# Performance work log

Hardware: AMD Instinct MI355X
Metric: run time of the kernel (lower is better)

Reference implementation:

```python
import jax, jax.numpy as jnp
import numpy as np
import math

S, D, H, DK, DV, FF = 128, 512, 8, 64, 64, 2048

def _pos_encoding(S, D):
    pos = jnp.arange(S, dtype=jnp.float32)[:, None]                      # [S,1]
    div = jnp.exp(jnp.arange(0, D, 2, dtype=jnp.float32) * (-math.log(10000.0) / D))
    pe = jnp.zeros((S, D), dtype=jnp.float32)
    pe = pe.at[:, 0::2].set(jnp.sin(pos * div))
    pe = pe.at[:, 1::2].set(jnp.cos(pos * div))
    return pe

def setup_inputs():
    key = jax.random.key(0)
    ks = jax.random.split(key, 16)
    B = 512
    return {
        'x':      jax.random.normal(ks[0], (B, S, D), dtype=jnp.float32),
        'emb_w':  jax.random.normal(ks[1], (D, D), dtype=jnp.float32) * 0.02,
        'emb_b':  jnp.zeros((D,), dtype=jnp.float32),
        'WQ':     jax.random.uniform(ks[2], (H, D, DK), dtype=jnp.float32) * 0.05,
        'WK':     jax.random.uniform(ks[3], (H, D, DK), dtype=jnp.float32) * 0.05,
        'WV':     jax.random.uniform(ks[4], (H, D, DV), dtype=jnp.float32) * 0.05,
        'WO':     jax.random.uniform(ks[5], (H * DV, D), dtype=jnp.float32) * 0.05,
        'norm_w': jnp.ones((S, D), dtype=jnp.float32),
        'norm_b': jnp.zeros((S, D), dtype=jnp.float32),
        'l1_w':   jax.random.normal(ks[6], (D, FF), dtype=jnp.float32) * 0.02,
        'l1_b':   jnp.zeros((FF,), dtype=jnp.float32),
        'l2_w':   jax.random.normal(ks[7], (FF, D), dtype=jnp.float32) * 0.02,
        'l2_b':   jnp.zeros((D,), dtype=jnp.float32),
        'fc_w':   jax.random.normal(ks[8], (256, 2), dtype=jnp.float32) * 0.05,
        'fc_b':   jnp.zeros((2,), dtype=jnp.float32),
    }

def reference(x, emb_w, emb_b, WQ, WK, WV, WO, norm_w, norm_b, l1_w, l1_b, l2_w, l2_b, fc_w, fc_b):
    B = x.shape[0]
    h = x @ emb_w + emb_b                                   # [B,S,D] embedding linear
    h = h + _pos_encoding(S, D)[None]                       # add sinusoidal PE
    # multi-head attention (all heads batched in one einsum instead of the per-head python loop)
    q = jnp.einsum('bsd,hdk->bhsk', h, WQ)                  # [B,H,S,DK]
    k = jnp.einsum('bsd,hdk->bhsk', h, WK)
    v = jnp.einsum('bsd,hdv->bhsv', h, WV)
    scores = jnp.einsum('bhsk,bhtk->bhst', q, k) / math.sqrt(DK)
    attn = jax.nn.softmax(scores, axis=-1)                  # [B,H,S,S]
    o = jnp.einsum('bhst,bhtv->bhsv', attn, v)              # [B,H,S,DV]
    o = jnp.transpose(o, (0, 2, 1, 3)).reshape(B, S, H * DV)  # concat heads
    o = o @ WO                                              # [B,S,D]
    # residual (dropout is identity in eval) + LayerNorm over (S, D)
    r = o + h
    mu = jnp.mean(r, axis=(1, 2), keepdims=True)
    var = jnp.mean(jnp.square(r - mu), axis=(1, 2), keepdims=True)
    r = (r - mu) * jax.lax.rsqrt(var + 1e-5) * norm_w + norm_b
    # FFN
    f = jax.nn.relu(r @ l1_w + l1_b) @ l2_w + l2_b          # [B,S,D]
    # MaxPool2d(16,16) over (S,D): [B,S,D] -> [B,S/16,D/16]
    p = f.reshape(B, S // 16, 16, D // 16, 16).max(axis=(2, 4))  # [B,8,32]
    p = p.reshape(B, 256)
    logits = p @ fc_w + fc_b                                # [B,2]
    return jax.nn.log_softmax(logits, axis=-1)
```

## Files before the change

kernel.cpp:

```cpp
#include <hip/hip_runtime.h>
#include <hip/hip_bf16.h>
#include <cstdint>
#include <math.h>

#define NB 512
#define NS 128
#define ND 512
#define NH 8
#define NDK 64
#define NFF 2048

typedef __attribute__((ext_vector_type(4))) float f32x4;
typedef __attribute__((ext_vector_type(8))) short s16x8;

#define AS1 __attribute__((address_space(1)))
#define AS3 __attribute__((address_space(3)))

__device__ __forceinline__ ushort f2b(float f) {
  __hip_bfloat16 h = __float2bfloat16(f);
  return *reinterpret_cast<ushort*>(&h);
}
__device__ __forceinline__ float b2f(ushort u) {
  __hip_bfloat16 h;
  *reinterpret_cast<ushort*>(&h) = u;
  return __bfloat162float(h);
}
__device__ __forceinline__ void gll16(const void* g, void* l) {
  __builtin_amdgcn_global_load_lds(
      (const AS1 unsigned int*)g,
      reinterpret_cast<AS3 unsigned int*>(reinterpret_cast<uintptr_t>(l)),
      16, 0, 0);
}

__global__ void conv_bf16(const float* __restrict__ in, ushort* __restrict__ out, int n4) {
  int i = blockIdx.x * blockDim.x + threadIdx.x;
  if (i >= n4) return;
  float4 v = *(const float4*)(in + (size_t)i * 4);
  ushort4 o;
  o.x = f2b(v.x); o.y = f2b(v.y); o.z = f2b(v.z); o.w = f2b(v.w);
  *(ushort4*)(out + (size_t)i * 4) = o;
}

__global__ void pack_t(const float* __restrict__ in, ushort* __restrict__ out, int R, int C) {
  int i = blockIdx.x * blockDim.x + threadIdx.x;
  if (i >= R * C) return;
  int r = i / C, c = i - r * C;
  out[(size_t)c * R + r] = f2b(in[i]);
}

__global__ void pack_qkv(const float* __restrict__ WQ, const float* __restrict__ WK,
                         const float* __restrict__ WV, ushort* __restrict__ out) {
  int i = blockIdx.x * blockDim.x + threadIdx.x;
  if (i >= NH * 192 * ND) return;
  int h = i / (192 * ND);
  int rem = i - h * (192 * ND);
  int n = rem / ND, d = rem - n * ND;
  size_t base = (size_t)h * ND * NDK + (size_t)d * NDK;
  float v;
  if (n < 64)       v = WQ[base + n] * 0.125f;
  else if (n < 128) v = WK[base + (n - 64)];
  else              v = WV[base + (n - 128)];
  out[i] = f2b(v);
}

__global__ void pe_build(float* __restrict__ pe) {
  int i = blockIdx.x * blockDim.x + threadIdx.x;
  if (i >= NS * ND) return;
  int s = i >> 9, d = i & 511;
  float e = expf((float)(d & ~1) * (-9.210340371976184f / 512.f));
  float ang = (float)s * e;
  pe[i] = (d & 1) ? cosf(ang) : sinf(ang);
}

template <int EPI>
__global__ __launch_bounds__(256, 2) void gemm_bf16(
    const ushort* __restrict__ A, const ushort* __restrict__ Bt,
    int M, int N, int K,
    ushort* __restrict__ Obf, float* __restrict__ Of,
    const float* __restrict__ bias, const float* __restrict__ pe,
    const ushort* __restrict__ res, float* __restrict__ stats,
    float* __restrict__ pool) {
  __shared__ __align__(16) ushort lA[2][4096];
  __shared__ __align__(16) ushort lB[2][4096];
  const int tid = threadIdx.x, lane = tid & 63, wid = tid >> 6;
  const int wr = wid >> 1, wc = wid & 1;
  const int lo = lane & 15, hi = lane >> 4;
  const int ntil = N >> 7;
  const int bm = blockIdx.x / ntil, bn = blockIdx.x - bm * ntil;
  const int m0 = bm << 7, n0 = bn << 7;
  const int rr = lane >> 2, cc = (lane & 3) << 3;

  f32x4 acc[4][4];
#pragma unroll
  for (int m = 0; m < 4; ++m)
#pragma unroll
    for (int n = 0; n < 4; ++n) acc[m][n] = (f32x4){0.f, 0.f, 0.f, 0.f};

  const int nk = K >> 5;
  for (int s = wid; s < 8; s += 4) {
    gll16(&A[(size_t)(m0 + s * 16 + rr) * K + cc], &lA[0][s * 512]);
    gll16(&Bt[(size_t)(n0 + s * 16 + rr) * K + cc], &lB[0][s * 512]);
  }
  __syncthreads();
  for (int t = 0; t < nk; ++t) {
    const int cur = t & 1;
    if (t + 1 < nk) {
      const int k0 = (t + 1) << 5;
      for (int s = wid; s < 8; s += 4) {
        gll16(&A[(size_t)(m0 + s * 16 + rr) * K + k0 + cc], &lA[cur ^ 1][s * 512]);
        gll16(&Bt[(size_t)(n0 + s * 16 + rr) * K + k0 + cc], &lB[cur ^ 1][s * 512]);
      }
    }
    s16x8 af[4], bfr[4];
#pragma unroll
    for (int m = 0; m < 4; ++m)
      af[m] = *(const s16x8*)&lA[cur][(wr * 64 + m * 16 + lo) * 32 + hi * 8];
#pragma unroll
    for (int n = 0; n < 4; ++n)
      bfr[n] = *(const s16x8*)&lB[cur][(wc * 64 + n * 16 + lo) * 32 + hi * 8];
#pragma unroll
    for (int m = 0; m < 4; ++m)
#pragma unroll
      for (int n = 0; n < 4; ++n)
        acc[m][n] = __builtin_amdgcn_mfma_f32_16x16x32_bf16(af[m], bfr[n], acc[m][n], 0, 0, 0);
    __syncthreads();
  }

  if constexpr (EPI == 0) {
#pragma unroll
    for (int m = 0; m < 4; ++m)
#pragma unroll
      for (int n = 0; n < 4; ++n) {
        const int col = n0 + wc * 64 + n * 16 + lo;
        const float bv = bias[col];
#pragma unroll
        for (int j = 0; j < 4; ++j) {
          const int row = m0 + wr * 64 + m * 16 + hi * 4 + j;
          const float v = acc[m][n][j] + bv + pe[((row & 127) << 9) + col];
          Obf[(size_t)row * N + col] = f2b(v);
        }
      }
  } else if constexpr (EPI == 1) {
    float s1 = 0.f, s2 = 0.f;
#pragma unroll
    for (int m = 0; m < 4; ++m)
#pragma unroll
      for (int n = 0; n < 4; ++n) {
        const int col = n0 + wc * 64 + n * 16 + lo;
#pragma unroll
        for (int j = 0; j < 4; ++j) {
          const int row = m0 + wr * 64 + m * 16 + hi * 4 + j;
          const float v = acc[m][n][j] + b2f(res[(size_t)row * 512 + col]);
          Of[(size_t)row * 512 + col] = v;
          s1 += v; s2 += v * v;
        }
      }
    s1 += __shfl_xor(s1, 1);  s2 += __shfl_xor(s2, 1);
    s1 += __shfl_xor(s1, 2);  s2 += __shfl_xor(s2, 2);
    s1 += __shfl_xor(s1, 4);  s2 += __shfl_xor(s2, 4);
    s1 += __shfl_xor(s1, 8);  s2 += __shfl_xor(s2, 8);
    s1 += __shfl_xor(s1, 16); s2 += __shfl_xor(s2, 16);
    s1 += __shfl_xor(s1, 32); s2 += __shfl_xor(s2, 32);
    if (lane == 0) {
      atomicAdd(&stats[bm * 2], s1);
      atomicAdd(&stats[bm * 2 + 1], s2);
    }
  } else if constexpr (EPI == 2) {
#pragma unroll
    for (int m = 0; m < 4; ++m)
#pragma unroll
      for (int n = 0; n < 4; ++n) {
        const int col = n0 + wc * 64 + n * 16 + lo;
        const float bv = bias[col];
#pragma unroll
        for (int j = 0; j < 4; ++j) {
          const int row = m0 + wr * 64 + m * 16 + hi * 4 + j;
          Obf[(size_t)row * N + col] = f2b(fmaxf(acc[m][n][j] + bv, 0.f));
        }
      }
  } else {
#pragma unroll
    for (int m = 0; m < 4; ++m)
#pragma unroll
      for (int n = 0; n < 4; ++n) {
        const int col = n0 + wc * 64 + n * 16 + lo;
        float fv = fmaxf(fmaxf(acc[m][n][0], acc[m][n][1]),
                         fmaxf(acc[m][n][2], acc[m][n][3])) + bias[col];
        fv = fmaxf(fv, __shfl_xor(fv, 1));
        fv = fmaxf(fv, __shfl_xor(fv, 2));
        fv = fmaxf(fv, __shfl_xor(fv, 4));
        fv = fmaxf(fv, __shfl_xor(fv, 8));
        fv = fmaxf(fv, __shfl_xor(fv, 16));
        fv = fmaxf(fv, __shfl_xor(fv, 32));
        if (lane == 0)
          pool[bm * 256 + (wr * 4 + m) * 32 + (bn * 8 + wc * 4 + n)] = fv;
      }
  }
}

__global__ __launch_bounds__(256, 2) void attn_fused(
    const ushort* __restrict__ h, const ushort* __restrict__ wqkvT,
    ushort* __restrict__ o) {
  __shared__ __align__(16) ushort smem[32768];
  ushort* uni = smem;
  ushort* kb = smem + 16384;
  ushort* vT = smem + 24576;
  float* redm = (float*)(smem + 16384);
  float* reds = redm + 256;

  const int tid = threadIdx.x, lane = tid & 63, wid = tid >> 6;
  const int wr = wid >> 1, wc = wid & 1;
  const int lo = lane & 15, hi = lane >> 4;
  const int bh = blockIdx.x;
  const int b = bh >> 3, hd = bh & 7;
  const ushort* hsrc = h + (size_t)b * (NS * ND);
  const ushort* wsrc = wqkvT + (size_t)hd * (192 * ND);
  const int rr = lane >> 2, cc = (lane & 3) << 3;

  f32x4 a1[4][6];
#pragma unroll
  for (int m = 0; m < 4; ++m)
#pragma unroll
    for (int n = 0; n < 6; ++n) a1[m][n] = (f32x4){0.f, 0.f, 0.f, 0.f};
  for (int t = 0; t < 16; ++t) {
    const int k0 = t << 5;
    for (int s = wid; s < 8; s += 4)
      gll16(&hsrc[(size_t)(s * 16 + rr) * ND + k0 + cc], &uni[s * 512]);
    for (int s = wid; s < 12; s += 4)
      gll16(&wsrc[(size_t)(s * 16 + rr) * ND + k0 + cc], &uni[4096 + s * 512]);
    __syncthreads();
    s16x8 af[4], bfr[6];
#pragma unroll
    for (int m = 0; m < 4; ++m)
      af[m] = *(const s16x8*)&uni[(wr * 64 + m * 16 + lo) * 32 + hi * 8];
#pragma unroll
    for (int n = 0; n < 6; ++n)
      bfr[n] = *(const s16x8*)&uni[4096 + (wc * 96 + n * 16 + lo) * 32 + hi * 8];
#pragma unroll
    for (int m = 0; m < 4; ++m)
#pragma unroll
      for (int n = 0; n < 6; ++n)
        a1[m][n] = __builtin_amdgcn_mfma_f32_16x16x32_bf16(af[m], bfr[n], a1[m][n], 0, 0, 0);
    __syncthreads();
  }
#pragma unroll
  for (int m = 0; m < 4; ++m)
#pragma unroll
    for (int n = 0; n < 6; ++n)
#pragma unroll
      for (int j = 0; j < 4; ++j) {
        const int row = wr * 64 + m * 16 + hi * 4 + j;
        const int c = wc * 96 + n * 16 + lo;
        const ushort v = f2b(a1[m][n][j]);
        if (c < 64) uni[row * 64 + c] = v;
        else if (c < 128) kb[row * 64 + (c - 64)] = v;
        else vT[(c - 128) * 128 + row] = v;
      }
  __syncthreads();

  f32x4 sc[4][4];
#pragma unroll
  for (int m = 0; m < 4; ++m)
#pragma unroll
    for (int n = 0; n < 4; ++n) sc[m][n] = (f32x4){0.f, 0.f, 0.f, 0.f};
#pragma unroll
  for (int kt = 0; kt < 2; ++kt) {
    s16x8 aq[4], bk[4];
#pragma unroll
    for (int m = 0; m < 4; ++m)
      aq[m] = *(const s16x8*)&uni[(wr * 64 + m * 16 + lo) * 64 + kt * 32 + hi * 8];
#pragma unroll
    for (int n = 0; n < 4; ++n)
      bk[n] = *(const s16x8*)&kb[(wc * 64 + n * 16 + lo) * 64 + kt * 32 + hi * 8];
#pragma unroll
    for (int m = 0; m < 4; ++m)
#pragma unroll
      for (int n = 0; n < 4; ++n)
        sc[m][n] = __builtin_amdgcn_mfma_f32_16x16x32_bf16(aq[m], bk[n], sc[m][n], 0, 0, 0);
  }
  __syncthreads();

  float rmax[4][4];
#pragma unroll
  for (int m = 0; m < 4; ++m)
#pragma unroll
    for (int j = 0; j < 4; ++j) {
      float v = fmaxf(fmaxf(sc[m][0][j], sc[m][1][j]), fmaxf(sc[m][2][j], sc[m][3][j]));
      v = fmaxf(v, __shfl_xor(v, 1));
      v = fmaxf(v, __shfl_xor(v, 2));
      v = fmaxf(v, __shfl_xor(v, 4));
      v = fmaxf(v, __shfl_xor(v, 8));
      rmax[m][j] = v;
    }
  if (lo == 0) {
#pragma unroll
    for (int m = 0; m < 4; ++m)
#pragma unroll
      for (int j = 0; j < 4; ++j)
        redm[wc * 128 + wr * 64 + m * 16 + hi * 4 + j] = rmax[m][j];
  }
  __syncthreads();
  float rsum[4][4];
#pragma unroll
  for (int m = 0; m < 4; ++m)
#pragma unroll
    for (int j = 0; j < 4; ++j) {
      const int row = wr * 64 + m * 16 + hi * 4 + j;
      const float mx = fmaxf(redm[row], redm[128 + row]);
      float s = 0.f;
#pragma unroll
      for (int n = 0; n < 4; ++n) {
        const float p = __expf(sc[m][n][j] - mx);
        uni[row * 128 + wc * 64 + n * 16 + lo] = f2b(p);
        s += p;
      }
      s += __shfl_xor(s, 1);
      s += __shfl_xor(s, 2);
      s += __shfl_xor(s, 4);
      s += __shfl_xor(s, 8);
      rsum[m][j] = s;
    }
  if (lo == 0) {
#pragma unroll
    for (int m = 0; m < 4; ++m)
#pragma unroll
      for (int j = 0; j < 4; ++j)
        reds[wc * 128 + wr * 64 + m * 16 + hi * 4 + j] = rsum[m][j];
  }
  __syncthreads();
  float inv[4][4];
#pragma unroll
  for (int m = 0; m < 4; ++m)
#pragma unroll
    for (int j = 0; j < 4; ++j) {
      const int row = wr * 64 + m * 16 + hi * 4 + j;
      inv[m][j] = 1.f / (reds[row] + reds[128 + row]);
    }

  f32x4 oa[4][2];
#pragma unroll
  for (int m = 0; m < 4; ++m)
#pragma unroll
    for (int n = 0; n < 2; ++n) oa[m][n] = (f32x4){0.f, 0.f, 0.f, 0.f};
#pragma unroll
  for (int kt = 0; kt < 4; ++kt) {
    s16x8 ap[4], bv[2];
#pragma unroll
    for (int m = 0; m < 4; ++m)
      ap[m] = *(const s16x8*)&uni[(wr * 64 + m * 16 + lo) * 128 + kt * 32 + hi * 8];
#pragma unroll
    for (int n = 0; n < 2; ++n)
      bv[n] = *(const s16x8*)&vT[(wc * 32 + n * 16 + lo) * 128 + kt * 32 + hi * 8];
#pragma unroll
    for (int m = 0; m < 4; ++m)
#pragma unroll
      for (int n = 0; n < 2; ++n)
        oa[m][n] = __builtin_amdgcn_mfma_f32_16x16x32_bf16(ap[m], bv[n], oa[m][n], 0, 0, 0);
  }
#pragma unroll
  for (int m = 0; m < 4; ++m)
#pragma unroll
    for (int n = 0; n < 2; ++n)
#pragma unroll
      for (int j = 0; j < 4; ++j) {
        const int row = wr * 64 + m * 16 + hi * 4 + j;
        const int c = wc * 32 + n * 16 + lo;
        o[((size_t)b * NS + row) * ND + hd * 64 + c] = f2b(oa[m][n][j] * inv[m][j]);
      }
}

__global__ void ln_apply(const float* __restrict__ r, const float* __restrict__ stats,
                         const float* __restrict__ nw, const float* __restrict__ nb,
                         ushort* __restrict__ rn) {
  int i = blockIdx.x * blockDim.x + threadIdx.x;
  int base = i << 2;
  if (base >= NB * NS * ND) return;
  int b = base >> 16;
  int sd = base & 65535;
  float mu = stats[2 * b] * (1.f / 65536.f);
  float var = stats[2 * b + 1] * (1.f / 65536.f) - mu * mu;
  float rs = rsqrtf(var + 1e-5f);
  float4 rv = *(const float4*)(r + base);
  float4 w = *(const float4*)(nw + sd);
  float4 bb = *(const float4*)(nb + sd);
  ushort4 ov;
  ov.x = f2b((rv.x - mu) * rs * w.x + bb.x);
  ov.y = f2b((rv.y - mu) * rs * w.y + bb.y);
  ov.z = f2b((rv.z - mu) * rs * w.z + bb.z);
  ov.w = f2b((rv.w - mu) * rs * w.w + bb.w);
  *(ushort4*)(rn + base) = ov;
}

__global__ void fc_logsoftmax(const float* __restrict__ p, const float* __restrict__ w,
                              const float* __restrict__ bias, float* __restrict__ out) {
  int b = blockIdx.x * blockDim.x + threadIdx.x;
  if (b >= NB) return;
  float l0 = bias[0], l1 = bias[1];
  const float* pr = p + b * 256;
  for (int k = 0; k < 256; ++k) {
    float pv = pr[k];
    l0 += pv * w[2 * k];
    l1 += pv * w[2 * k + 1];
  }
  float mx = fmaxf(l0, l1);
  float lse = mx + logf(expf(l0 - mx) + expf(l1 - mx));
  out[2 * b] = l0 - lse;
  out[2 * b + 1] = l1 - lse;
}

extern "C" void kernel_launch(void* const* d_in, const int* in_sizes, int n_in,
                              void* d_out, int out_size, void* d_ws, size_t ws_size,
                              hipStream_t stream) {
  const float* x      = (const float*)d_in[0];
  const float* emb_w  = (const float*)d_in[1];
  const float* emb_b  = (const float*)d_in[2];
  const float* WQ     = (const float*)d_in[3];
  const float* WK     = (const float*)d_in[4];
  const float* WV     = (const float*)d_in[5];
  const float* WO     = (const float*)d_in[6];
  const float* norm_w = (const float*)d_in[7];
  const float* norm_b = (const float*)d_in[8];
  const float* l1_w   = (const float*)d_in[9];
  const float* l1_b   = (const float*)d_in[10];
  const float* l2_w   = (const float*)d_in[11];
  const float* l2_b   = (const float*)d_in[12];
  const float* fc_w   = (const float*)d_in[13];
  const float* fc_b   = (const float*)d_in[14];
  float* out = (float*)d_out;
  char* ws = (char*)d_ws;

  constexpr size_t MB = 1ull << 20;
  ushort* xb   = (ushort*)(ws + 0);
  ushort* hbuf = (ushort*)(ws + 64 * MB);
  ushort* obuf = (ushort*)(ws + 128 * MB);
  float*  rbuf = (float*)(ws + 192 * MB);
  ushort* f1   = (ushort*)(ws + 0);
  ushort* rnb  = (ushort*)(ws + 320 * MB);
  char* wb = ws + 384 * MB;
  ushort* embT  = (ushort*)(wb);
  ushort* woT   = (ushort*)(wb + 524288);
  ushort* l1T   = (ushort*)(wb + 1048576);
  ushort* l2T   = (ushort*)(wb + 3145728);
  ushort* wqkvT = (ushort*)(wb + 5242880);
  float*  peb   = (float*)(wb + 6815744);
  float*  stats = (float*)(wb + 7077888);
  float*  poolb = (float*)(wb + 7086080);

  hipMemsetAsync(stats, 0, NB * 2 * sizeof(float), stream);

  conv_bf16<<<32768, 256, 0, stream>>>(x, xb, NB * NS * ND / 4);
  pe_build<<<256, 256, 0, stream>>>(peb);
  pack_t<<<1024, 256, 0, stream>>>(emb_w, embT, 512, 512);
  pack_t<<<1024, 256, 0, stream>>>(WO, woT, 512, 512);
  pack_t<<<4096, 256, 0, stream>>>(l1_w, l1T, 512, 2048);
  pack_t<<<4096, 256, 0, stream>>>(l2_w, l2T, 2048, 512);
  pack_qkv<<<3072, 256, 0, stream>>>(WQ, WK, WV, wqkvT);

  gemm_bf16<0><<<2048, 256, 0, stream>>>(xb, embT, NB * NS, ND, ND,
                                         hbuf, nullptr, emb_b, peb, nullptr, nullptr, nullptr);
  attn_fused<<<NB * NH, 256, 0, stream>>>(hbuf, wqkvT, obuf);
  gemm_bf16<1><<<2048, 256, 0, stream>>>(obuf, woT, NB * NS, ND, ND,
                                         nullptr, rbuf, nullptr, nullptr, hbuf, stats, nullptr);
  ln_apply<<<32768, 256, 0, stream>>>(rbuf, stats, norm_w, norm_b, rnb);
  gemm_bf16<2><<<8192, 256, 0, stream>>>(rnb, l1T, NB * NS, NFF, ND,
                                         f1, nullptr, l1_b, nullptr, nullptr, nullptr, nullptr);
  gemm_bf16<3><<<2048, 256, 0, stream>>>(f1, l2T, NB * NS, ND, NFF,
                                         nullptr, nullptr, l2_b, nullptr, nullptr, nullptr, poolb);
  fc_logsoftmax<<<2, 256, 0, stream>>>(poolb, fc_w, fc_b, out);
}
```

Measured before the change: 1.054 ms.

## Split fused attention into QKV GEMM plus lightweight attention core kernel

The per-(batch,head) QKV projection moves out of the attention kernel into a separate full-tile GEMM with a new epilogue. That epilogue scatters Q, K and transposed V into per-head bf16 buffers in global memory. The attention kernel then only loads these tiles into XOR-swizzled shared memory, computes the scores with each wave owning full rows, and does the softmax without cross-wave reductions. This aims for better MFMA efficiency in the projection and higher occupancy in attention, at the cost of an extra global round trip for Q/K/V and reshuffled workspace aliasing.

```diff
diff --git a/kernel.cpp b/kernel.cpp
--- a/kernel.cpp
+++ b/kernel.cpp
@@ -178,7 +178,7 @@
           Obf[(size_t)row * N + col] = f2b(fmaxf(acc[m][n][j] + bv, 0.f));
         }
       }
-  } else {
+  } else if constexpr (EPI == 3) {
 #pragma unroll
     for (int m = 0; m < 4; ++m)
 #pragma unroll
@@ -195,177 +195,154 @@
         if (lane == 0)
           pool[bm * 256 + (wr * 4 + m) * 32 + (bn * 8 + wc * 4 + n)] = fv;
       }
-  }
-}
-
-__global__ __launch_bounds__(256, 2) void attn_fused(
-    const ushort* __restrict__ h, const ushort* __restrict__ wqkvT,
-    ushort* __restrict__ o) {
-  __shared__ __align__(16) ushort smem[32768];
-  ushort* uni = smem;
-  ushort* kb = smem + 16384;
-  ushort* vT = smem + 24576;
-  float* redm = (float*)(smem + 16384);
-  float* reds = redm + 256;
-
+  } else {
+    ushort* kbp = (ushort*)Of;
+    ushort* vtp = (ushort*)pool;
+#pragma unroll
+    for (int m = 0; m < 4; ++m)
+#pragma unroll
+      for (int n = 0; n < 4; ++n) {
+        const int cn0 = n0 + wc * 64 + n * 16;
+        const int h = cn0 / 192;
+        const int rem = cn0 - h * 192;
+        const int kind = rem >> 6;
+        const int idx = (rem & 63) + lo;
+#pragma unroll
+        for (int j = 0; j < 4; ++j) {
+          const int row = m0 + wr * 64 + m * 16 + hi * 4 + j;
+          const size_t hb = (size_t)((row >> 7) * 8 + h) * 8192;
+          const ushort v = f2b(acc[m][n][j]);
+          if (kind == 0)      Obf[hb + (row & 127) * 64 + idx] = v;
+          else if (kind == 1) kbp[hb + (row & 127) * 64 + idx] = v;
+          else                vtp[hb + (size_t)idx * 128 + (row & 127)] = v;
+        }
+      }
+  }
+}
+
+__global__ __launch_bounds__(256, 3) void attn_core(
+    const ushort* __restrict__ qb, const ushort* __restrict__ kb,
+    const ushort* __restrict__ vtb, ushort* __restrict__ o) {
+  __shared__ __align__(16) ushort smem[24576];
   const int tid = threadIdx.x, lane = tid & 63, wid = tid >> 6;
-  const int wr = wid >> 1, wc = wid & 1;
   const int lo = lane & 15, hi = lane >> 4;
   const int bh = blockIdx.x;
-  const int b = bh >> 3, hd = bh & 7;
-  const ushort* hsrc = h + (size_t)b * (NS * ND);
-  const ushort* wsrc = wqkvT + (size_t)hd * (192 * ND);
-  const int rr = lane >> 2, cc = (lane & 3) << 3;
-
-  f32x4 a1[4][6];
-#pragma unroll
-  for (int m = 0; m < 4; ++m)
-#pragma unroll
-    for (int n = 0; n < 6; ++n) a1[m][n] = (f32x4){0.f, 0.f, 0.f, 0.f};
-  for (int t = 0; t < 16; ++t) {
-    const int k0 = t << 5;
-    for (int s = wid; s < 8; s += 4)
-      gll16(&hsrc[(size_t)(s * 16 + rr) * ND + k0 + cc], &uni[s * 512]);
-    for (int s = wid; s < 12; s += 4)
-      gll16(&wsrc[(size_t)(s * 16 + rr) * ND + k0 + cc], &uni[4096 + s * 512]);
-    __syncthreads();
-    s16x8 af[4], bfr[6];
-#pragma unroll
-    for (int m = 0; m < 4; ++m)
-      af[m] = *(const s16x8*)&uni[(wr * 64 + m * 16 + lo) * 32 + hi * 8];
-#pragma unroll
-    for (int n = 0; n < 6; ++n)
-      bfr[n] = *(const s16x8*)&uni[4096 + (wc * 96 + n * 16 + lo) * 32 + hi * 8];
-#pragma unroll
-    for (int m = 0; m < 4; ++m)
-#pragma unroll
-      for (int n = 0; n < 6; ++n)
-        a1[m][n] = __builtin_amdgcn_mfma_f32_16x16x32_bf16(af[m], bfr[n], a1[m][n], 0, 0, 0);
-    __syncthreads();
-  }
-#pragma unroll
-  for (int m = 0; m < 4; ++m)
-#pragma unroll
-    for (int n = 0; n < 6; ++n)
-#pragma unroll
-      for (int j = 0; j < 4; ++j) {
-        const int row = wr * 64 + m * 16 + hi * 4 + j;
-        const int c = wc * 96 + n * 16 + lo;
-        const ushort v = f2b(a1[m][n][j]);
-        if (c < 64) uni[row * 64 + c] = v;
-        else if (c < 128) kb[row * 64 + (c - 64)] = v;
-        else vT[(c - 128) * 128 + row] = v;
-      }
+  const size_t base = (size_t)bh * 8192;
+
+#pragma unroll
+  for (int i = 0; i < 4; ++i) {
+    const int Lb = (wid * 4 + i) * 64;
+    const int L = Lb + lane;
+    {
+      const int r = L >> 3, c = L & 7;
+      gll16(&qb[base + r * 64 + ((c ^ (r & 7)) << 3)], &smem[Lb * 8]);
+      gll16(&kb[base + r * 64 + ((c ^ (r & 7)) << 3)], &smem[8192 + Lb * 8]);
+    }
+    {
+      const int r = L >> 4, c = L & 15;
+      gll16(&vtb[base + r * 128 + ((c ^ (r & 15)) << 3)], &smem[16384 + Lb * 8]);
+    }
+  }
   __syncthreads();
 
-  f32x4 sc[4][4];
-#pragma unroll
-  for (int m = 0; m < 4; ++m)
-#pragma unroll
-    for (int n = 0; n < 4; ++n) sc[m][n] = (f32x4){0.f, 0.f, 0.f, 0.f};
+  f32x4 sc[2][8];
+#pragma unroll
+  for (int m = 0; m < 2; ++m)
+#pragma unroll
+    for (int n = 0; n < 8; ++n) sc[m][n] = (f32x4){0.f, 0.f, 0.f, 0.f};
 #pragma unroll
   for (int kt = 0; kt < 2; ++kt) {
-    s16x8 aq[4], bk[4];
-#pragma unroll
-    for (int m = 0; m < 4; ++m)
-      aq[m] = *(const s16x8*)&uni[(wr * 64 + m * 16 + lo) * 64 + kt * 32 + hi * 8];
-#pragma unroll
-    for (int n = 0; n < 4; ++n)
-      bk[n] = *(const s16x8*)&kb[(wc * 64 + n * 16 + lo) * 64 + kt * 32 + hi * 8];
-#pragma unroll
-    for (int m = 0; m < 4; ++m)
-#pragma unroll
-      for (int n = 0; n < 4; ++n)
+    s16x8 aq[2], bk[8];
+#pragma unroll
+    for (int m = 0; m < 2; ++m) {
+      const int row = wid * 32 + m * 16 + lo;
+      aq[m] = *(const s16x8*)&smem[row * 64 + (((kt * 4 + hi) ^ (row & 7)) << 3)];
+    }
+#pragma unroll
+    for (int n = 0; n < 8; ++n) {
+      const int kr = n * 16 + lo;
+      bk[n] = *(const s16x8*)&smem[8192 + kr * 64 + (((kt * 4 + hi) ^ (kr & 7)) << 3)];
+    }
+#pragma unroll
+    for (int m = 0; m < 2; ++m)
+#pragma unroll
+      for (int n = 0; n < 8; ++n)
         sc[m][n] = __builtin_amdgcn_mfma_f32_16x16x32_bf16(aq[m], bk[n], sc[m][n], 0, 0, 0);
   }
   __syncthreads();
 
-  float rmax[4][4];
-#pragma unroll
-  for (int m = 0; m < 4; ++m)
+  float inv[2][4];
+#pragma unroll
+  for (int m = 0; m < 2; ++m)
 #pragma unroll
     for (int j = 0; j < 4; ++j) {
-      float v = fmaxf(fmaxf(sc[m][0][j], sc[m][1][j]), fmaxf(sc[m][2][j], sc[m][3][j]));
-      v = fmaxf(v, __shfl_xor(v, 1));
-      v = fmaxf(v, __shfl_xor(v, 2));
-      v = fmaxf(v, __shfl_xor(v, 4));
-      v = fmaxf(v, __shfl_xor(v, 8));
-      rmax[m][j] = v;
-    }
-  if (lo == 0) {
-#pragma unroll
-    for (int m = 0; m < 4; ++m)
-#pragma unroll
-      for (int j = 0; j < 4; ++j)
-        redm[wc * 128 + wr * 64 + m * 16 + hi * 4 + j] = rmax[m][j];
-  }
-  __syncthreads();
-  float rsum[4][4];
-#pragma unroll
-  for (int m = 0; m < 4; ++m)
-#pragma unroll
-    for (int j = 0; j < 4; ++j) {
-      const int row = wr * 64 + m * 16 + hi * 4 + j;
-      const float mx = fmaxf(redm[row], redm[128 + row]);
+      float mx = sc[m][0][j];
+#pragma unroll
+      for (int n = 1; n < 8; ++n) mx = fmaxf(mx, sc[m][n][j]);
+      mx = fmaxf(mx, __shfl_xor(mx, 1));
+      mx = fmaxf(mx, __shfl_xor(mx, 2));
+      mx = fmaxf(mx, __shfl_xor(mx, 4));
+      mx = fmaxf(mx, __shfl_xor(mx, 8));
       float s = 0.f;
 #pragma unroll
-      for (int n = 0; n < 4; ++n) {
+      for (int n = 0; n < 8; ++n) {
         const float p = __expf(sc[m][n][j] - mx);
-        uni[row * 128 + wc * 64 + n * 16 + lo] = f2b(p);
+        sc[m][n][j] = p;
         s += p;
       }
       s += __shfl_xor(s, 1);
       s += __shfl_xor(s, 2);
       s += __shfl_xor(s, 4);
       s += __shfl_xor(s, 8);
-      rsum[m][j] = s;
-    }
-  if (lo == 0) {
-#pragma unroll
-    for (int m = 0; m < 4; ++m)
-#pragma unroll
-      for (int j = 0; j < 4; ++j)
-        reds[wc * 128 + wr * 64 + m * 16 + hi * 4 + j] = rsum[m][j];
-  }
+      inv[m][j] = 1.f / s;
+    }
+#pragma unroll
+  for (int m = 0; m < 2; ++m)
+#pragma unroll
+    for (int n = 0; n < 8; ++n)
+#pragma unroll
+      for (int j = 0; j < 4; ++j) {
+        const int row = wid * 32 + m * 16 + hi * 4 + j;
+        const int col = n * 16 + lo;
+        smem[row * 128 + ((((col >> 3) ^ (row & 15)) << 3) | (col & 7))] =
+            f2b(sc[m][n][j]);
+      }
   __syncthreads();
-  float inv[4][4];
-#pragma unroll
-  for (int m = 0; m < 4; ++m)
-#pragma unroll
-    for (int j = 0; j < 4; ++j) {
-      const int row = wr * 64 + m * 16 + hi * 4 + j;
-      inv[m][j] = 1.f / (reds[row] + reds[128 + row]);
-    }
-
-  f32x4 oa[4][2];
-#pragma unroll
-  for (int m = 0; m < 4; ++m)
-#pragma unroll
-    for (int n = 0; n < 2; ++n) oa[m][n] = (f32x4){0.f, 0.f, 0.f, 0.f};
+
+  f32x4 oa[2][4];
+#pragma unroll
+  for (int m = 0; m < 2; ++m)
+#pragma unroll
+    for (int n = 0; n < 4; ++n) oa[m][n] = (f32x4){0.f, 0.f, 0.f, 0.f};
 #pragma unroll
   for (int kt = 0; kt < 4; ++kt) {
-    s16x8 ap[4], bv[2];
-#pragma unroll
-    for (int m = 0; m < 4; ++m)
-      ap[m] = *(const s16x8*)&uni[(wr * 64 + m * 16 + lo) * 128 + kt * 32 + hi * 8];
-#pragma unroll
-    for (int n = 0; n < 2; ++n)
-      bv[n] = *(const s16x8*)&vT[(wc * 32 + n * 16 + lo) * 128 + kt * 32 + hi * 8];
-#pragma unroll
-    for (int m = 0; m < 4; ++m)
-#pragma unroll
-      for (int n = 0; n < 2; ++n)
+    s16x8 ap[2], bv[4];
+#pragma unroll
+    for (int m = 0; m < 2; ++m) {
+      const int row = wid * 32 + m * 16 + lo;
+      ap[m] = *(const s16x8*)&smem[row * 128 + (((kt * 4 + hi) ^ (row & 15)) << 3)];
+    }
+#pragma unroll
+    for (int n = 0; n < 4; ++n) {
+      const int vr = n * 16 + lo;
+      bv[n] = *(const s16x8*)&smem[16384 + vr * 128 + (((kt * 4 + hi) ^ (vr & 15)) << 3)];
+    }
+#pragma unroll
+    for (int m = 0; m < 2; ++m)
+#pragma unroll
+      for (int n = 0; n < 4; ++n)
         oa[m][n] = __builtin_amdgcn_mfma_f32_16x16x32_bf16(ap[m], bv[n], oa[m][n], 0, 0, 0);
   }
-#pragma unroll
-  for (int m = 0; m < 4; ++m)
-#pragma unroll
-    for (int n = 0; n < 2; ++n)
+  const int b = bh >> 3, hd = bh & 7;
+#pragma unroll
+  for (int m = 0; m < 2; ++m)
+#pragma unroll
+    for (int n = 0; n < 4; ++n)
 #pragma unroll
       for (int j = 0; j < 4; ++j) {
-        const int row = wr * 64 + m * 16 + hi * 4 + j;
-        const int c = wc * 32 + n * 16 + lo;
-        o[((size_t)b * NS + row) * ND + hd * 64 + c] = f2b(oa[m][n][j] * inv[m][j]);
+        const int row = wid * 32 + m * 16 + hi * 4 + j;
+        const int col = n * 16 + lo;
+        o[(size_t)b * 65536 + row * 512 + hd * 64 + col] = f2b(oa[m][n][j] * inv[m][j]);
       }
 }
 
@@ -430,12 +407,15 @@
   char* ws = (char*)d_ws;
 
   constexpr size_t MB = 1ull << 20;
-  ushort* xb   = (ushort*)(ws + 0);
-  ushort* hbuf = (ushort*)(ws + 64 * MB);
-  ushort* obuf = (ushort*)(ws + 128 * MB);
-  float*  rbuf = (float*)(ws + 192 * MB);
-  ushort* f1   = (ushort*)(ws + 0);
-  ushort* rnb  = (ushort*)(ws + 320 * MB);
+  ushort* xb    = (ushort*)(ws + 0);
+  ushort* qb    = (ushort*)(ws + 0);
+  ushort* hbuf  = (ushort*)(ws + 64 * MB);
+  ushort* kbuf  = (ushort*)(ws + 128 * MB);
+  ushort* obuf  = (ushort*)(ws + 192 * MB);
+  ushort* vtb   = (ushort*)(ws + 256 * MB);
+  float*  rbuf  = (float*)(ws + 256 * MB);
+  ushort* rnb   = (ushort*)(ws + 64 * MB);
+  ushort* f1    = (ushort*)(ws + 128 * MB);
   char* wb = ws + 384 * MB;
   ushort* embT  = (ushort*)(wb);
   ushort* woT   = (ushort*)(wb + 524288);
@@ -444,7 +424,7 @@
   ushort* wqkvT = (ushort*)(wb + 5242880);
   float*  peb   = (float*)(wb + 6815744);
   float*  stats = (float*)(wb + 7077888);
-  float*  poolb = (float*)(wb + 7086080);
+  float*  poolb = (float*)(wb + 7081984);
 
   hipMemsetAsync(stats, 0, NB * 2 * sizeof(float), stream);
 
@@ -458,7 +438,10 @@
 
   gemm_bf16<0><<<2048, 256, 0, stream>>>(xb, embT, NB * NS, ND, ND,
                                          hbuf, nullptr, emb_b, peb, nullptr, nullptr, nullptr);
-  attn_fused<<<NB * NH, 256, 0, stream>>>(hbuf, wqkvT, obuf);
+  gemm_bf16<4><<<6144, 256, 0, stream>>>(hbuf, wqkvT, NB * NS, NH * 192, ND,
+                                         qb, (float*)kbuf, nullptr, nullptr, nullptr, nullptr,
+                                         (float*)vtb);
+  attn_core<<<NB * NH, 256, 0, stream>>>(qb, kbuf, vtb, obuf);
   gemm_bf16<1><<<2048, 256, 0, stream>>>(obuf, woT, NB * NS, ND, ND,
                                          nullptr, rbuf, nullptr, nullptr, hbuf, stats, nullptr);
   ln_apply<<<32768, 256, 0, stream>>>(rbuf, stats, norm_w, norm_b, rnb);
```

Result: no change. 1.062 ms (+0.8%).
